# Optimization experiments

Hardware: AMD Instinct MI355X
Metric: run time of the kernel (lower is better)

## Reference

```python
import jax, jax.numpy as jnp
import numpy as np

PATCH_SIZES = [4, 8, 16]
B, S, D, H = 32, 1000, 64, 512


def setup_inputs() -> dict:
    key = jax.random.key(0)
    ks = jax.random.split(key, 8)
    inp = {"x": jax.random.normal(ks[0], (B, S, D), dtype=jnp.float32)}
    for i, p in enumerate(PATCH_SIZES):
        fan_in = p * D
        inp[f"W{i}"] = jax.random.normal(ks[1 + 2 * i], (H, fan_in), dtype=jnp.float32) / np.sqrt(fan_in).astype(np.float32)
        inp[f"b{i}"] = jax.random.normal(ks[2 + 2 * i], (H,), dtype=jnp.float32) * 0.01
    inp["pos"] = jax.random.normal(ks[7], (1, 1000, H), dtype=jnp.float32)
    return inp


def reference(x, W0, b0, W1, b1, W2, b2, pos):
    Ws = [W0, W1, W2]
    bs = [b0, b1, b2]
    batch, seq_len, d = x.shape
    min_len = seq_len - max(PATCH_SIZES) + 1  # all scales truncated to this
    embs = []
    for p, W, b in zip(PATCH_SIZES, Ws, bs):
        # sliding windows, stride 1, only the first min_len windows are kept
        idx = jnp.arange(min_len)[:, None] + jnp.arange(p)[None, :]  # (min_len, p)
        win = x[:, idx, :]  # (batch, min_len, p, d) -- im2col gather
        # torch Linear on flattened [time, feature] patch: W[h, t*d + f]
        Wk = W.reshape(-1, p, d)  # (H, p, d)
        embs.append(jnp.einsum('blpd,hpd->blh', win, Wk) + b)
    out = jnp.stack(embs, axis=1).mean(axis=1)  # mean over scales
    return out + pos[:, :min_len, :]
```

## Files before the change

### kernel.cpp

```cpp
#include <hip/hip_runtime.h>
#include <stdint.h>

typedef unsigned short u16;
typedef __attribute__((ext_vector_type(8))) short bf16x8;
typedef __attribute__((ext_vector_type(8))) u16  u16x8;
typedef __attribute__((ext_vector_type(4))) float f32x4;

static constexpr int BATCH  = 32;
static constexpr int SEQ    = 1000;
static constexpr int DIM    = 64;
static constexpr int HOUT   = 512;
static constexpr int MINLEN = 985;
static constexpr int KTOT   = 1024;
static constexpr int AROWS  = 144;
static constexpr int BBUF   = 128 * 32;

static constexpr size_t XB_OFF   = 0;
static constexpr size_t WF_OFF   = 4u << 20;
static constexpr size_t BE_OFF   = 5u << 20;
static constexpr int    XB_TOTAL = 2048000 + 4096;

__device__ inline u16 f2bf(float f) {
  union { float f; uint32_t u; } v; v.f = f;
  uint32_t r = v.u + 0x7fffu + ((v.u >> 16) & 1u);
  return (u16)(r >> 16);
}

__global__ void pe_prep(const float* __restrict__ x,
                        const float* __restrict__ W0, const float* __restrict__ W1,
                        const float* __restrict__ W2, const float* __restrict__ b0,
                        const float* __restrict__ b1, const float* __restrict__ b2,
                        u16* __restrict__ xb, u16* __restrict__ Wf,
                        float* __restrict__ beff) {
  int bid = blockIdx.x;
  if (bid < 1002) {
    int i = (bid * 256 + threadIdx.x) * 8;
    u16x8 o;
    if (i < 2048000) {
      const float4* p = (const float4*)(x + i);
      float4 a = p[0], c = p[1];
      o[0] = f2bf(a.x); o[1] = f2bf(a.y); o[2] = f2bf(a.z); o[3] = f2bf(a.w);
      o[4] = f2bf(c.x); o[5] = f2bf(c.y); o[6] = f2bf(c.z); o[7] = f2bf(c.w);
    } else {
      o = (u16x8)(0);
    }
    *(u16x8*)(xb + i) = o;
  } else {
    int i = (bid - 1002) * 256 + threadIdx.x;
    if (i < HOUT * KTOT) {
      int h = i >> 10, j = i & 1023;
      float e = W2[i];
      if (j < 512) e += W1[(h << 9) + j];
      if (j < 256) e += W0[(h << 8) + j];
      Wf[i] = f2bf(e * (1.0f / 3.0f));
    } else {
      int h = i - HOUT * KTOT;
      beff[h] = (b0[h] + b1[h] + b2[h]) * (1.0f / 3.0f);
    }
  }
}

__device__ inline void gload_lds16(const void* g, void* l) {
  __builtin_amdgcn_global_load_lds(
      (const __attribute__((address_space(1))) uint32_t*)g,
      (__attribute__((address_space(3))) uint32_t*)l, 16, 0, 0);
}

__global__ __launch_bounds__(256, 4) void pe_gemm(
    const u16* __restrict__ xb, const u16* __restrict__ Wf,
    const float* __restrict__ beff, const float* __restrict__ pos,
    float* __restrict__ out) {
  __shared__ u16 ldsA[AROWS * 64];
  __shared__ u16 ldsB[2][BBUF];

  const int t    = threadIdx.x;
  const int w    = t >> 6;
  const int lane = t & 63;
  const int b    = blockIdx.z;
  const int l0   = blockIdx.y * 128;
  const int n0   = blockIdx.x * 128;
  const int wr   = w >> 1;
  const int wc   = w & 1;
  const int lr   = lane & 15;
  const int g    = lane >> 4;

  const int sra = lane >> 3;
  const int sca = ((lane & 7) ^ sra) * 8;
  const int srb = lane >> 2;
  const int scb = ((lane & 3) ^ ((lane >> 3) & 3)) * 8;

  const u16* Ab = xb + b * (SEQ * DIM) + l0 * 64;
  const u16* Bb = Wf + (size_t)n0 * KTOT;

  #pragma unroll
  for (int i = 0; i < 4; ++i) {
    int c = w * 4 + i;
    gload_lds16(Ab + (c * 8 + sra) * 64 + sca, &ldsA[c * 512]);
  }
  if (w < 2) {
    int c = 16 + w;
    gload_lds16(Ab + (c * 8 + sra) * 64 + sca, &ldsA[c * 512]);
  }
  #pragma unroll
  for (int i = 0; i < 2; ++i) {
    int c = w * 2 + i;
    gload_lds16(Bb + (size_t)(c * 16 + srb) * KTOT + scb, &ldsB[0][c * 512]);
  }
  __syncthreads();

  f32x4 acc[4][4] = {};
  int bc = 0;

  #pragma unroll 2
  for (int kt = 0; kt < 32; ++kt) {
    if (kt < 31) {
      #pragma unroll
      for (int i = 0; i < 2; ++i) {
        int c = w * 2 + i;
        gload_lds16(Bb + (size_t)(c * 16 + srb) * KTOT + (kt + 1) * 32 + scb,
                    &ldsB[bc ^ 1][c * 512]);
      }
    }
    bf16x8 aF[4], bF[4];
    #pragma unroll
    for (int m = 0; m < 4; ++m) {
      int r = wr * 64 + m * 16 + lr + (kt >> 1);
      int s = (((kt & 1) * 4 + g) ^ (r & 7));
      aF[m] = *(const bf16x8*)&ldsA[r * 64 + s * 8];
    }
    #pragma unroll
    for (int n = 0; n < 4; ++n) {
      int r = wc * 64 + n * 16 + lr;
      int s = g ^ ((r >> 1) & 3);
      bF[n] = *(const bf16x8*)&ldsB[bc][r * 32 + s * 8];
    }
    #pragma unroll
    for (int m = 0; m < 4; ++m)
      #pragma unroll
      for (int n = 0; n < 4; ++n)
        acc[m][n] = __builtin_amdgcn_mfma_f32_16x16x32_bf16(aF[m], bF[n], acc[m][n], 0, 0, 0);
    __syncthreads();
    bc ^= 1;
  }

  #pragma unroll
  for (int n = 0; n < 4; ++n) {
    const int h  = n0 + wc * 64 + n * 16 + lr;
    const float bv = beff[h];
    #pragma unroll
    for (int m = 0; m < 4; ++m) {
      const int rowb = l0 + wr * 64 + m * 16 + (g << 2);
      #pragma unroll
      for (int r = 0; r < 4; ++r) {
        const int l = rowb + r;
        if (l < MINLEN) {
          out[((size_t)b * MINLEN + l) * HOUT + h] =
              acc[m][n][r] + bv + pos[(size_t)l * HOUT + h];
        }
      }
    }
  }
}

extern "C" void kernel_launch(void* const* d_in, const int* in_sizes, int n_in,
                              void* d_out, int out_size, void* d_ws, size_t ws_size,
                              hipStream_t stream) {
  const float* x   = (const float*)d_in[0];
  const float* W0  = (const float*)d_in[1];
  const float* b0  = (const float*)d_in[2];
  const float* W1  = (const float*)d_in[3];
  const float* b1  = (const float*)d_in[4];
  const float* W2  = (const float*)d_in[5];
  const float* b2  = (const float*)d_in[6];
  const float* pos = (const float*)d_in[7];
  float* out = (float*)d_out;

  char* ws  = (char*)d_ws;
  u16*  xbf = (u16*)(ws + XB_OFF);
  u16*  Wf  = (u16*)(ws + WF_OFF);
  float* be = (float*)(ws + BE_OFF);

  hipLaunchKernelGGL(pe_prep, dim3(3052), dim3(256), 0, stream,
                     x, W0, W1, W2, b0, b1, b2, xbf, Wf, be);
  hipLaunchKernelGGL(pe_gemm, dim3(HOUT / 128, 8, BATCH), dim3(256), 0, stream,
                     xbf, Wf, be, pos, out);
}
```

Before: 56.40 us.

## Pre-pack weights in MFMA fragment order and load B directly to registers

The prep kernel now writes the fused weight matrix in a packed layout that matches the per-lane MFMA B-fragment order, using vectorized 8-wide loads and stores. The GEMM drops the double-buffered LDS staging of B and the per-k-step barrier, loading B fragments straight from global memory into registers, ping-ponged across two k-steps. This removes LDS traffic and sync for B, but each wave now issues its own global loads of B (shared across waves only through cache), and load latency is hidden only by the register double-buffer.

```diff
diff --git a/kernel.cpp b/kernel.cpp
--- a/kernel.cpp
+++ b/kernel.cpp
@@ -13,7 +13,6 @@
 static constexpr int MINLEN = 985;
 static constexpr int KTOT   = 1024;
 static constexpr int AROWS  = 144;
-static constexpr int BBUF   = 128 * 32;
 
 static constexpr size_t XB_OFF   = 0;
 static constexpr size_t WF_OFF   = 4u << 20;
@@ -30,7 +29,7 @@
                         const float* __restrict__ W0, const float* __restrict__ W1,
                         const float* __restrict__ W2, const float* __restrict__ b0,
                         const float* __restrict__ b1, const float* __restrict__ b2,
-                        u16* __restrict__ xb, u16* __restrict__ Wf,
+                        u16* __restrict__ xb, u16* __restrict__ Wp,
                         float* __restrict__ beff) {
   int bid = blockIdx.x;
   if (bid < 1002) {
@@ -45,18 +44,32 @@
       o = (u16x8)(0);
     }
     *(u16x8*)(xb + i) = o;
+  } else if (bid < 1258) {
+    int j  = (bid - 1002) * 256 + threadIdx.x;
+    int h  = j >> 7;
+    int kc = j & 127;
+    float v[8];
+    const float4* w2 = (const float4*)(W2 + h * 1024 + kc * 8);
+    float4 a = w2[0], c = w2[1];
+    v[0]=a.x; v[1]=a.y; v[2]=a.z; v[3]=a.w; v[4]=c.x; v[5]=c.y; v[6]=c.z; v[7]=c.w;
+    if (kc < 64) {
+      const float4* w1 = (const float4*)(W1 + h * 512 + kc * 8);
+      float4 d = w1[0], e = w1[1];
+      v[0]+=d.x; v[1]+=d.y; v[2]+=d.z; v[3]+=d.w; v[4]+=e.x; v[5]+=e.y; v[6]+=e.z; v[7]+=e.w;
+    }
+    if (kc < 32) {
+      const float4* w0 = (const float4*)(W0 + h * 256 + kc * 8);
+      float4 d = w0[0], e = w0[1];
+      v[0]+=d.x; v[1]+=d.y; v[2]+=d.z; v[3]+=d.w; v[4]+=e.x; v[5]+=e.y; v[6]+=e.z; v[7]+=e.w;
+    }
+    u16x8 o;
+    #pragma unroll
+    for (int e = 0; e < 8; ++e) o[e] = f2bf(v[e] * (1.0f / 3.0f));
+    size_t dst = ((size_t)(h >> 4) * 32 + (kc >> 2)) * 512 + (kc & 3) * 128 + (h & 15) * 8;
+    *(u16x8*)(Wp + dst) = o;
   } else {
-    int i = (bid - 1002) * 256 + threadIdx.x;
-    if (i < HOUT * KTOT) {
-      int h = i >> 10, j = i & 1023;
-      float e = W2[i];
-      if (j < 512) e += W1[(h << 9) + j];
-      if (j < 256) e += W0[(h << 8) + j];
-      Wf[i] = f2bf(e * (1.0f / 3.0f));
-    } else {
-      int h = i - HOUT * KTOT;
-      beff[h] = (b0[h] + b1[h] + b2[h]) * (1.0f / 3.0f);
-    }
+    int h = (bid - 1258) * 256 + threadIdx.x;
+    if (h < HOUT) beff[h] = (b0[h] + b1[h] + b2[h]) * (1.0f / 3.0f);
   }
 }
 
@@ -67,11 +80,10 @@
 }
 
 __global__ __launch_bounds__(256, 4) void pe_gemm(
-    const u16* __restrict__ xb, const u16* __restrict__ Wf,
+    const u16* __restrict__ xb, const u16* __restrict__ Wp,
     const float* __restrict__ beff, const float* __restrict__ pos,
     float* __restrict__ out) {
   __shared__ u16 ldsA[AROWS * 64];
-  __shared__ u16 ldsB[2][BBUF];
 
   const int t    = threadIdx.x;
   const int w    = t >> 6;
@@ -86,11 +98,9 @@
 
   const int sra = lane >> 3;
   const int sca = ((lane & 7) ^ sra) * 8;
-  const int srb = lane >> 2;
-  const int scb = ((lane & 3) ^ ((lane >> 3) & 3)) * 8;
 
   const u16* Ab = xb + b * (SEQ * DIM) + l0 * 64;
-  const u16* Bb = Wf + (size_t)n0 * KTOT;
+  const u16* Bp = Wp + ((size_t)((n0 >> 4) + wc * 4) * 32) * 512 + lane * 8;
 
   #pragma unroll
   for (int i = 0; i < 4; ++i) {
@@ -101,47 +111,48 @@
     int c = 16 + w;
     gload_lds16(Ab + (c * 8 + sra) * 64 + sca, &ldsA[c * 512]);
   }
+
+  bf16x8 bA[4], bB[4];
   #pragma unroll
-  for (int i = 0; i < 2; ++i) {
-    int c = w * 2 + i;
-    gload_lds16(Bb + (size_t)(c * 16 + srb) * KTOT + scb, &ldsB[0][c * 512]);
-  }
+  for (int n = 0; n < 4; ++n)
+    bA[n] = *(const bf16x8*)(Bp + (size_t)(n * 32) * 512);
+
   __syncthreads();
 
   f32x4 acc[4][4] = {};
-  int bc = 0;
+  const int rbase = wr * 64 + lr;
 
-  #pragma unroll 2
-  for (int kt = 0; kt < 32; ++kt) {
-    if (kt < 31) {
-      #pragma unroll
-      for (int i = 0; i < 2; ++i) {
-        int c = w * 2 + i;
-        gload_lds16(Bb + (size_t)(c * 16 + srb) * KTOT + (kt + 1) * 32 + scb,
-                    &ldsB[bc ^ 1][c * 512]);
-      }
+  #define A_READS(kt_, aF_)                                                   \
+    _Pragma("unroll")                                                         \
+    for (int m = 0; m < 4; ++m) {                                             \
+      int r = rbase + m * 16 + ((kt_) >> 1);                                  \
+      int s = ((((kt_) & 1) << 2) + g) ^ (r & 7);                             \
+      aF_[m] = *(const bf16x8*)&ldsA[r * 64 + s * 8];                         \
     }
-    bf16x8 aF[4], bF[4];
-    #pragma unroll
-    for (int m = 0; m < 4; ++m) {
-      int r = wr * 64 + m * 16 + lr + (kt >> 1);
-      int s = (((kt & 1) * 4 + g) ^ (r & 7));
-      aF[m] = *(const bf16x8*)&ldsA[r * 64 + s * 8];
-    }
-    #pragma unroll
-    for (int n = 0; n < 4; ++n) {
-      int r = wc * 64 + n * 16 + lr;
-      int s = g ^ ((r >> 1) & 3);
-      bF[n] = *(const bf16x8*)&ldsB[bc][r * 32 + s * 8];
-    }
-    #pragma unroll
-    for (int m = 0; m < 4; ++m)
-      #pragma unroll
-      for (int n = 0; n < 4; ++n)
-        acc[m][n] = __builtin_amdgcn_mfma_f32_16x16x32_bf16(aF[m], bF[n], acc[m][n], 0, 0, 0);
-    __syncthreads();
-    bc ^= 1;
+  #define B_LOADS(kt_, dst_)                                                  \
+    _Pragma("unroll")                                                         \
+    for (int n = 0; n < 4; ++n)                                               \
+      dst_[n] = *(const bf16x8*)(Bp + (size_t)(n * 32 + (kt_)) * 512);
+  #define MFMAS(aF_, bF_)                                                     \
+    _Pragma("unroll")                                                         \
+    for (int m = 0; m < 4; ++m)                                               \
+      _Pragma("unroll")                                                       \
+      for (int n = 0; n < 4; ++n)                                             \
+        acc[m][n] = __builtin_amdgcn_mfma_f32_16x16x32_bf16(aF_[m], bF_[n],   \
+                                                            acc[m][n], 0, 0, 0);
+
+  for (int kt = 0; kt < 32; kt += 2) {
+    bf16x8 aF[4];
+    if (kt + 1 < 32) { B_LOADS(kt + 1, bB); }
+    A_READS(kt, aF);
+    MFMAS(aF, bA);
+    if (kt + 2 < 32) { B_LOADS(kt + 2, bA); }
+    A_READS(kt + 1, aF);
+    MFMAS(aF, bB);
   }
+  #undef A_READS
+  #undef B_LOADS
+  #undef MFMAS
 
   #pragma unroll
   for (int n = 0; n < 4; ++n) {
@@ -177,11 +188,11 @@
 
   char* ws  = (char*)d_ws;
   u16*  xbf = (u16*)(ws + XB_OFF);
-  u16*  Wf  = (u16*)(ws + WF_OFF);
+  u16*  Wp  = (u16*)(ws + WF_OFF);
   float* be = (float*)(ws + BE_OFF);
 
-  hipLaunchKernelGGL(pe_prep, dim3(3052), dim3(256), 0, stream,
-                     x, W0, W1, W2, b0, b1, b2, xbf, Wf, be);
+  hipLaunchKernelGGL(pe_prep, dim3(1260), dim3(256), 0, stream,
+                     x, W0, W1, W2, b0, b1, b2, xbf, Wp, be);
   hipLaunchKernelGGL(pe_gemm, dim3(HOUT / 128, 8, BATCH), dim3(256), 0, stream,
-                     xbf, Wf, be, pos, out);
+                     xbf, Wp, be, pos, out);
 }
```

Result: faster. 54.79 us (-2.9%).
